# Kernel optimization log

Measured on AMD Instinct MI355X. Metric: run time of the kernel, lower is better.

Reference implementation:

```python
import jax, jax.numpy as jnp
import numpy as np

B = 2048          # batch (vmapped samples)
STEPS = 64        # hardcoded scan length in module
H = 64            # hidden_size
W = 128           # width_size
NZ = 32           # noise_size (control_size)
INZ = 32          # initial_noise_size
D = 8             # data_size


def lipswish(x):
    return 0.909 * jax.nn.silu(x)


def _mlp3(x, W0, b0, W1, b1, W2, b2, act, final_act):
    # eqx.nn.MLP with depth=2: in->width, width->width, width->out
    h = act(x @ W0.T + b0)
    h = act(h @ W1.T + b1)
    return final_act(h @ W2.T + b2)


def setup_inputs() -> dict:
    key = jax.random.key(0)
    ks = jax.random.split(key, 32)

    def lin(k, out_d, in_d):
        lim = 1.0 / np.sqrt(in_d)
        kw, kb = jax.random.split(k)
        Wm = jax.random.uniform(kw, (out_d, in_d), minval=-lim, maxval=lim, dtype=jnp.float32)
        bv = jax.random.uniform(kb, (out_d,), minval=-lim, maxval=lim, dtype=jnp.float32)
        return Wm, bv

    Wi0, bi0 = lin(ks[0], W, INZ)
    Wi1, bi1 = lin(ks[1], W, W)
    Wi2, bi2 = lin(ks[2], H, W)

    Wv0, bv0 = lin(ks[3], W, H + 1)
    Wv1, bv1 = lin(ks[4], W, W)
    Wv2, bv2 = lin(ks[5], H, W)
    scale_v = jax.random.uniform(ks[6], (H,), minval=0.9, maxval=1.1, dtype=jnp.float32)

    Wc0, bc0 = lin(ks[7], W, H + 1)
    Wc1, bc1 = lin(ks[8], W, W)
    Wc2, bc2 = lin(ks[9], H * NZ, W)
    scale_c = jax.random.uniform(ks[10], (H, NZ), minval=0.9, maxval=1.1, dtype=jnp.float32)

    Wr, br = lin(ks[11], D, H)

    ts = jnp.arange(STEPS + 1, dtype=jnp.float32)
    init_noise = jax.random.normal(ks[12], (B, INZ), dtype=jnp.float32)
    bm = jax.random.normal(ks[13], (B, STEPS, NZ), dtype=jnp.float32)

    return dict(ts=ts, init_noise=init_noise, bm=bm,
                Wi0=Wi0, bi0=bi0, Wi1=Wi1, bi1=bi1, Wi2=Wi2, bi2=bi2,
                scale_v=scale_v, Wv0=Wv0, bv0=bv0, Wv1=Wv1, bv1=bv1, Wv2=Wv2, bv2=bv2,
                scale_c=scale_c, Wc0=Wc0, bc0=bc0, Wc1=Wc1, bc1=bc1, Wc2=Wc2, bc2=bc2,
                Wr=Wr, br=br)


def reference(ts, init_noise, bm,
              Wi0, bi0, Wi1, bi1, Wi2, bi2,
              scale_v, Wv0, bv0, Wv1, bv1, Wv2, bv2,
              scale_c, Wc0, bc0, Wc1, bc1, Wc2, bc2,
              Wr, br):
    t0 = ts[0]
    dt = jnp.float32(1.0)  # dt0 hardcoded in module
    sqrt_dt = jnp.sqrt(dt)

    # initial MLP (relu hidden, identity final): noise -> y0 [B,H]
    y0 = _mlp3(init_noise, Wi0, bi0, Wi1, bi1, Wi2, bi2, jax.nn.relu, lambda x: x)

    bm_t = jnp.transpose(bm, (1, 0, 2))  # [STEPS, B, NZ]
    idx = jnp.arange(STEPS, dtype=jnp.float32)

    def step(y, xs):
        i, bm_i = xs
        t = t0 + i * dt
        tcol = jnp.broadcast_to(jnp.reshape(t, (1, 1)), (y.shape[0], 1))
        inp = jnp.concatenate([tcol, y], axis=1)  # [B, H+1]
        # drift vector field
        drift = scale_v * _mlp3(inp, Wv0, bv0, Wv1, bv1, Wv2, bv2, lipswish, jnp.tanh)
        # controlled vector field: [B, H, NZ]
        diff = scale_c * _mlp3(inp, Wc0, bc0, Wc1, bc1, Wc2, bc2, lipswish, jnp.tanh).reshape(-1, H, NZ)
        y1 = y + drift * dt + jnp.einsum('bhn,bn->bh', diff, bm_i * sqrt_dt)
        return y1, y1

    _, ys = jax.lax.scan(step, y0, (idx, bm_t), length=STEPS, unroll=8)  # ys [STEPS,B,H]
    out = jnp.einsum('tbh,dh->tbd', ys, Wr) + br  # readout per step
    return jnp.transpose(out, (1, 0, 2))  # [B, STEPS, D]
```

## Files before the change

kernel.cpp:

```cpp
#include <hip/hip_runtime.h>
#include <stdint.h>
#include <stddef.h>


typedef __attribute__((ext_vector_type(8))) short bf16x8;
typedef __attribute__((ext_vector_type(4))) float f32x4;
typedef __attribute__((ext_vector_type(2))) float f32x2;
typedef __attribute__((ext_vector_type(4))) int   i32x4;

#define BB 16
#define NWG 256

#define WS_WI0 0
#define WS_WI1 8192
#define WS_WI2 40960
#define WS_WV0 57344
#define WS_WV1 73728
#define WS_WV2 106496
#define WS_WC0 122880
#define WS_WC1 139264
#define WS_WC2 172032
#define WS_TV0 696320
#define WS_TC0 696832
#define WS_XCHG 700416
#define WS_FLAG 2273280

#define LD_WV0 0
#define LD_WV1 16384
#define LD_WC0 49152
#define LD_WC1 65536
#define LD_YBF 98304
#define LD_H1V 100352
#define LD_H1C 104448
#define LD_H2V 108544
#define LD_H2C 112640
#define LD_Y   116736
#define LD_DB  121088
#define LD_BM  125440
#define LD_BSC 127552
#define LD_BEV 135744
#define LD_BEC 136256
#define LD_BV1 136768
#define LD_BC1 137280
#define LD_BV2 137792
#define LD_SV  138048
#define LD_WR  138304
#define LD_BR  140480
#define LDS_TOTAL 140512

__device__ __forceinline__ short f2bf(float f) {
  uint32_t u = __builtin_bit_cast(uint32_t, f);
  uint32_t r = (u + 0x7fffu + ((u >> 16) & 1u)) >> 16;
  return (short)r;
}
__device__ __forceinline__ float bf2f(short s) {
  uint32_t u = ((uint32_t)(uint16_t)s) << 16;
  return __builtin_bit_cast(float, u);
}
__device__ __forceinline__ float tanh_fast(float x) {
  float e = __builtin_amdgcn_exp2f(x * 2.8853900817779268f);
  return __builtin_fmaf(-2.f, __builtin_amdgcn_rcpf(e + 1.f), 1.f);
}
__device__ __forceinline__ float lipswish(float x) {
  float s = __builtin_amdgcn_rcpf(1.f + __builtin_amdgcn_exp2f(-1.4426950408889634f * x));
  return 0.909f * x * s;
}
__device__ __forceinline__ float red16(float x) {
  int v;
  v = __builtin_amdgcn_update_dpp(0, __builtin_bit_cast(int, x), 0xB1, 0xF, 0xF, true);
  x += __builtin_bit_cast(float, v);
  v = __builtin_amdgcn_update_dpp(0, __builtin_bit_cast(int, x), 0x4E, 0xF, 0xF, true);
  x += __builtin_bit_cast(float, v);
  v = __builtin_amdgcn_update_dpp(0, __builtin_bit_cast(int, x), 0x141, 0xF, 0xF, true);
  x += __builtin_bit_cast(float, v);
  v = __builtin_amdgcn_update_dpp(0, __builtin_bit_cast(int, x), 0x140, 0xF, 0xF, true);
  x += __builtin_bit_cast(float, v);
  return x;
}
__device__ __forceinline__ float red4(float x) {
  int v;
  v = __builtin_amdgcn_update_dpp(0, __builtin_bit_cast(int, x), 0xB1, 0xF, 0xF, true);
  x += __builtin_bit_cast(float, v);
  v = __builtin_amdgcn_update_dpp(0, __builtin_bit_cast(int, x), 0x4E, 0xF, 0xF, true);
  x += __builtin_bit_cast(float, v);
  return x;
}
__device__ __forceinline__ void write_act(char* buf, int m, int k, short v) {
  int addr = ((k >> 5) << 10) + (m + ((k >> 3) & 3) * 16) * 16 + ((k & 7) << 1);
  *(short*)(buf + addr) = v;
}

template<int KF>
__device__ __forceinline__ f32x4 gemm_tile(const char* abase, const char* bbase, int lane) {
  f32x4 acc = {0.f, 0.f, 0.f, 0.f};
#pragma unroll
  for (int k = 0; k < KF; k++) {
    bf16x8 a = *(const bf16x8*)(abase + k * 1024 + lane * 16);
    bf16x8 b = *(const bf16x8*)(bbase + k * 1024 + lane * 16);
    acc = __builtin_amdgcn_mfma_f32_16x16x32_bf16(a, b, acc, 0, 0, 0);
  }
  return acc;
}

__global__ __launch_bounds__(256) void prep_kernel(
    const float* Wi0, const float* Wi1, const float* Wi2,
    const float* Wv0, const float* Wv1, const float* Wv2,
    const float* Wc0, const float* Wc1, const float* Wc2, char* ws) {
  int gid = blockIdx.x * 256 + threadIdx.x;
  if (gid < 512) ((unsigned*)(ws + WS_FLAG))[gid] = 0;
  if (gid < 680 * 64) {
    int frag = gid >> 6, lane = gid & 63;
    const float* src; int start, KI, srcK, c0;
    if      (frag < 8)   { src = Wi0; start = 0;   KI = 1; srcK = 32;  c0 = 0; }
    else if (frag < 40)  { src = Wi1; start = 8;   KI = 4; srcK = 128; c0 = 0; }
    else if (frag < 56)  { src = Wi2; start = 40;  KI = 4; srcK = 128; c0 = 0; }
    else if (frag < 72)  { src = Wv0; start = 56;  KI = 2; srcK = 65;  c0 = 1; }
    else if (frag < 104) { src = Wv1; start = 72;  KI = 4; srcK = 128; c0 = 0; }
    else if (frag < 120) { src = Wv2; start = 104; KI = 4; srcK = 128; c0 = 0; }
    else if (frag < 136) { src = Wc0; start = 120; KI = 2; srcK = 65;  c0 = 1; }
    else if (frag < 168) { src = Wc1; start = 136; KI = 4; srcK = 128; c0 = 0; }
    else                 { src = Wc2; start = 168; KI = 4; srcK = 128; c0 = 0; }
    int rel = frag - start;
    int nt = rel / KI, ki = rel % KI;
    int n16 = lane & 15, quad = lane >> 4;
    const float* s = src + (nt * 16 + n16) * srcK + c0 + ki * 32 + quad * 8;
    bf16x8 v;
#pragma unroll
    for (int j = 0; j < 8; j++) v[j] = f2bf(s[j]);
    *(bf16x8*)(ws + (size_t)frag * 1024 + lane * 16) = v;
  } else {
    int i = gid - 680 * 64;
    if (i < 128)      ((float*)(ws + WS_TV0))[i] = Wv0[i * 65];
    else if (i < 256) ((float*)(ws + WS_TC0))[i - 128] = Wc0[(i - 128) * 65];
  }
}

__global__ __launch_bounds__(512, 2)
void sde_kernel(
    const float* ts, const float* init_noise, const float* bm,
    const float* bi0, const float* bi1, const float* bi2,
    const float* bv0, const float* bv1, const float* bv2, const float* scale_v,
    const float* bc0, const float* bc1, const float* bc2, const float* scale_c,
    const float* Wr, const float* br,
    char* ws, float* out) {
  extern __shared__ __align__(16) char lds[];
  const int tid  = threadIdx.x;
  const int lane = tid & 63;
  const int wv   = tid >> 6;
  const int nl   = lane & 15;
  const int quad = lane >> 4;
  const int bid  = blockIdx.x;
  const int ro   = (bid >> 3) & 1;
  const int pid  = ((bid >> 4) << 3) | (bid & 7);
  const int b0   = pid * BB;
  const int hbase = ro << 5;
  const char* wc2 = ws + WS_WC2 + (size_t)(ro * 64 + wv * 8) * 4096;
  char* xch = ws + WS_XCHG;
  unsigned* flags = (unsigned*)(ws + WS_FLAG);
  const int myflag = (pid << 1) | ro;
  const int paflag = (pid << 1) | (1 - ro);

  bf16x8 vf0 = {}, vf1 = {}, vf2 = {}, vf3 = {};
  if (wv < 2) {
    const char* vb = ws + WS_WV2 + (size_t)(ro * 2 + wv) * 4096;
    vf0 = *(const bf16x8*)(vb +    0 + lane * 16);
    vf1 = *(const bf16x8*)(vb + 1024 + lane * 16);
    vf2 = *(const bf16x8*)(vb + 2048 + lane * 16);
    vf3 = *(const bf16x8*)(vb + 3072 + lane * 16);
  }
  float tvq = 0.f, bbq = 0.f;
  if (tid >= 256) {
    int j = tid - 256;
    if (j < 128) { tvq = ((const float*)(ws + WS_TV0))[j];       bbq = bv0[j]; }
    else         { tvq = ((const float*)(ws + WS_TC0))[j - 128]; bbq = bc0[j - 128]; }
  }

  {
    const i32x4* s0 = (const i32x4*)(ws + WS_WV0);
    const i32x4* s1 = (const i32x4*)(ws + WS_WC0);
    i32x4* d0 = (i32x4*)(lds + LD_WV0);
    i32x4* d1 = (i32x4*)(lds + LD_WC0);
    for (int j = tid; j < 3072; j += 512) { d0[j] = s0[j]; d1[j] = s1[j]; }
  }
  for (int j = tid; j < 2048; j += 512) {
    uint32_t u = (uint32_t)(uint16_t)f2bf(bc2[j]) |
                 ((uint32_t)(uint16_t)f2bf(scale_c[j]) << 16);
    ((uint32_t*)(lds + LD_BSC))[j] = u;
  }
  if (tid < 128)      { ((float*)(lds + LD_BV1))[tid] = bv1[tid];
                        ((float*)(lds + LD_BC1))[tid] = bc1[tid]; }
  else if (tid < 192) { int k = tid - 128; ((float*)(lds + LD_BV2))[k] = bv2[k];
                        ((float*)(lds + LD_SV))[k] = scale_v[k]; }
  else if (tid < 200) { int k = tid - 192; ((float*)(lds + LD_BR))[k] = br[k]; }
  { int dd = tid >> 6, k = tid & 63;
    ((float*)(lds + LD_WR))[dd * 68 + k] = Wr[dd * 64 + k]; }
  { int m = tid >> 5, k = tid & 31;
    write_act(lds + LD_YBF, m, k, f2bf(init_noise[(b0 + m) * 32 + k])); }
  __syncthreads();

  { f32x4 acc = gemm_tile<1>(lds + LD_YBF, ws + WS_WI0 + wv * 1024, lane);
    int col = wv * 16 + nl; float bias = bi0[col];
#pragma unroll
    for (int r = 0; r < 4; r++)
      write_act(lds + LD_H1V, quad * 4 + r, col, f2bf(fmaxf(0.f, acc[r] + bias))); }
  __syncthreads();
  { f32x4 acc = gemm_tile<4>(lds + LD_H1V, ws + WS_WI1 + wv * 4096, lane);
    int col = wv * 16 + nl; float bias = bi1[col];
#pragma unroll
    for (int r = 0; r < 4; r++)
      write_act(lds + LD_H2V, quad * 4 + r, col, f2bf(fmaxf(0.f, acc[r] + bias))); }
  __syncthreads();
  if (wv < 4) {
    f32x4 acc = gemm_tile<4>(lds + LD_H2V, ws + WS_WI2 + wv * 4096, lane);
    int col = wv * 16 + nl; float bias = bi2[col];
#pragma unroll
    for (int r = 0; r < 4; r++)
      ((float*)(lds + LD_Y))[(quad * 4 + r) * 68 + col] = acc[r] + bias;
  }
  __syncthreads();

  const float ts0 = ts[0];
  for (int e = tid; e < 1024; e += 512) {
    int row = e >> 6, k = e & 63;
    write_act(lds + LD_YBF, row, k, f2bf(((float*)(lds + LD_Y))[row * 68 + k]));
  }
  ((float*)(lds + LD_BM))[(tid >> 5) * 33 + (tid & 31)] =
      bm[((size_t)(b0 + (tid >> 5)) * 64 + 0) * 32 + (tid & 31)];
  if (tid >= 256) {
    int j = tid - 256; float v = bbq + ts0 * tvq;
    if (j < 128) ((float*)(lds + LD_BEV))[j] = v;
    else         ((float*)(lds + LD_BEC))[j - 128] = v;
  }
  __syncthreads();

  for (int step = 0; step < 64; step++) {
    {
      int col = wv * 16 + nl;
      f32x4 av = gemm_tile<2>(lds + LD_YBF, lds + LD_WV0 + wv * 2048, lane);
      f32x4 ac = gemm_tile<2>(lds + LD_YBF, lds + LD_WC0 + wv * 2048, lane);
      float bv = ((float*)(lds + LD_BEV))[col];
      float bc = ((float*)(lds + LD_BEC))[col];
#pragma unroll
      for (int r = 0; r < 4; r++) {
        write_act(lds + LD_H1V, quad * 4 + r, col, f2bf(lipswish(av[r] + bv)));
        write_act(lds + LD_H1C, quad * 4 + r, col, f2bf(lipswish(ac[r] + bc)));
      }
    }
    __syncthreads();
    bf16x8 bE0 = *(const bf16x8*)(wc2 +    0 + lane * 16);
    bf16x8 bE1 = *(const bf16x8*)(wc2 + 1024 + lane * 16);
    bf16x8 bE2 = *(const bf16x8*)(wc2 + 2048 + lane * 16);
    bf16x8 bE3 = *(const bf16x8*)(wc2 + 3072 + lane * 16);
    bf16x8 bO0 = *(const bf16x8*)(wc2 + 4096 +    0 + lane * 16);
    bf16x8 bO1 = *(const bf16x8*)(wc2 + 4096 + 1024 + lane * 16);
    bf16x8 bO2 = *(const bf16x8*)(wc2 + 4096 + 2048 + lane * 16);
    bf16x8 bO3 = *(const bf16x8*)(wc2 + 4096 + 3072 + lane * 16);
    {
      int col = wv * 16 + nl;
      f32x4 av = gemm_tile<4>(lds + LD_H1V, lds + LD_WV1 + wv * 4096, lane);
      f32x4 ac = gemm_tile<4>(lds + LD_H1C, lds + LD_WC1 + wv * 4096, lane);
      float bv = ((float*)(lds + LD_BV1))[col];
      float bc = ((float*)(lds + LD_BC1))[col];
#pragma unroll
      for (int r = 0; r < 4; r++) {
        write_act(lds + LD_H2V, quad * 4 + r, col, f2bf(lipswish(av[r] + bv)));
        write_act(lds + LD_H2C, quad * 4 + r, col, f2bf(lipswish(ac[r] + bc)));
      }
    }
    __syncthreads();
    float bm_next = 0.f;
    if (step + 1 < 64)
      bm_next = bm[((size_t)(b0 + (tid >> 5)) * 64 + (step + 1)) * 32 + (tid & 31)];
    if (wv < 2) {
      f32x4 acc = {0.f, 0.f, 0.f, 0.f};
      acc = __builtin_amdgcn_mfma_f32_16x16x32_bf16(
          *(const bf16x8*)(lds + LD_H2V +    0 + lane * 16), vf0, acc, 0, 0, 0);
      acc = __builtin_amdgcn_mfma_f32_16x16x32_bf16(
          *(const bf16x8*)(lds + LD_H2V + 1024 + lane * 16), vf1, acc, 0, 0, 0);
      acc = __builtin_amdgcn_mfma_f32_16x16x32_bf16(
          *(const bf16x8*)(lds + LD_H2V + 2048 + lane * 16), vf2, acc, 0, 0, 0);
      acc = __builtin_amdgcn_mfma_f32_16x16x32_bf16(
          *(const bf16x8*)(lds + LD_H2V + 3072 + lane * 16), vf3, acc, 0, 0, 0);
      int col = (ro * 2 + wv) * 16 + nl;
      float bias = ((float*)(lds + LD_BV2))[col];
      float sv   = ((float*)(lds + LD_SV))[col];
#pragma unroll
      for (int r = 0; r < 4; r++)
        ((float*)(lds + LD_DB))[(quad * 4 + r) * 68 + col] = sv * tanh_fast(acc[r] + bias);
    }
    {
      bf16x8 a0f = *(const bf16x8*)(lds + LD_H2C +    0 + lane * 16);
      bf16x8 a1f = *(const bf16x8*)(lds + LD_H2C + 1024 + lane * 16);
      bf16x8 a2f = *(const bf16x8*)(lds + LD_H2C + 2048 + lane * 16);
      bf16x8 a3f = *(const bf16x8*)(lds + LD_H2C + 3072 + lane * 16);
      const float* bmp = (const float*)(lds + LD_BM);
      float bmr00 = bmp[(quad * 4 + 0) * 33 + nl];
      float bmr01 = bmp[(quad * 4 + 1) * 33 + nl];
      float bmr02 = bmp[(quad * 4 + 2) * 33 + nl];
      float bmr03 = bmp[(quad * 4 + 3) * 33 + nl];
      float bmr10 = bmp[(quad * 4 + 0) * 33 + 16 + nl];
      float bmr11 = bmp[(quad * 4 + 1) * 33 + 16 + nl];
      float bmr12 = bmp[(quad * 4 + 2) * 33 + 16 + nl];
      float bmr13 = bmp[(quad * 4 + 3) * 33 + 16 + nl];
      const uint32_t* bscp = (const uint32_t*)(lds + LD_BSC) + (ro * 64 + wv * 8) * 16 + nl;
      float ps0, ps1, ps2, ps3;

#define DIFF_PAIR(P)                                                          \
      {                                                     \
        f32x4 acc = {0.f, 0.f, 0.f, 0.f};                                     \
        acc = __builtin_amdgcn_mfma_f32_16x16x32_bf16(a0f, bE0, acc, 0, 0, 0);\
        acc = __builtin_amdgcn_mfma_f32_16x16x32_bf16(a1f, bE1, acc, 0, 0, 0);\
        acc = __builtin_amdgcn_mfma_f32_16x16x32_bf16(a2f, bE2, acc, 0, 0, 0);\
        acc = __builtin_amdgcn_mfma_f32_16x16x32_bf16(a3f, bE3, acc, 0, 0, 0);\
        if ((P) < 3) {                                                        \
          bE0 = *(const bf16x8*)(wc2 + (2*(P)+2)*4096 +    0 + lane*16);      \
          bE1 = *(const bf16x8*)(wc2 + (2*(P)+2)*4096 + 1024 + lane*16);      \
          bE2 = *(const bf16x8*)(wc2 + (2*(P)+2)*4096 + 2048 + lane*16);      \
          bE3 = *(const bf16x8*)(wc2 + (2*(P)+2)*4096 + 3072 + lane*16);      \
        }                                                                     \
        uint32_t bsc = bscp[(2*(P))*16];                                      \
        float bc2v = bf2f((short)(bsc & 0xffffu));                            \
        float scv  = bf2f((short)(bsc >> 16));                                \
        ps0 = tanh_fast(acc[0] + bc2v) * scv * bmr00;                         \
        ps1 = tanh_fast(acc[1] + bc2v) * scv * bmr01;                         \
        ps2 = tanh_fast(acc[2] + bc2v) * scv * bmr02;                         \
        ps3 = tanh_fast(acc[3] + bc2v) * scv * bmr03;                         \
      }                                                                       \
      {                                                    \
        f32x4 acc = {0.f, 0.f, 0.f, 0.f};                                     \
        acc = __builtin_amdgcn_mfma_f32_16x16x32_bf16(a0f, bO0, acc, 0, 0, 0);\
        acc = __builtin_amdgcn_mfma_f32_16x16x32_bf16(a1f, bO1, acc, 0, 0, 0);\
        acc = __builtin_amdgcn_mfma_f32_16x16x32_bf16(a2f, bO2, acc, 0, 0, 0);\
        acc = __builtin_amdgcn_mfma_f32_16x16x32_bf16(a3f, bO3, acc, 0, 0, 0);\
        if ((P) < 3) {                                                        \
          bO0 = *(const bf16x8*)(wc2 + (2*(P)+3)*4096 +    0 + lane*16);      \
          bO1 = *(const bf16x8*)(wc2 + (2*(P)+3)*4096 + 1024 + lane*16);      \
          bO2 = *(const bf16x8*)(wc2 + (2*(P)+3)*4096 + 2048 + lane*16);      \
          bO3 = *(const bf16x8*)(wc2 + (2*(P)+3)*4096 + 3072 + lane*16);      \
        }                                                                     \
        uint32_t bsc = bscp[(2*(P)+1)*16];                                    \
        float bc2v = bf2f((short)(bsc & 0xffffu));                            \
        float scv  = bf2f((short)(bsc >> 16));                                \
        ps0 += tanh_fast(acc[0] + bc2v) * scv * bmr10;                        \
        ps1 += tanh_fast(acc[1] + bc2v) * scv * bmr11;                        \
        ps2 += tanh_fast(acc[2] + bc2v) * scv * bmr12;                        \
        ps3 += tanh_fast(acc[3] + bc2v) * scv * bmr13;                        \
        ps0 = red16(ps0); ps1 = red16(ps1); ps2 = red16(ps2); ps3 = red16(ps3);\
        if (nl < 4) {                                                         \
          int row = quad * 4 + nl;                                            \
          float s = (nl == 0) ? ps0 : (nl == 1) ? ps1 : (nl == 2) ? ps2 : ps3;\
          ((float*)(lds + LD_Y))[row * 68 + (hbase + (wv << 2) + (P))] += s;  \
        }                                                                     \
      }

      DIFF_PAIR(0)
      DIFF_PAIR(1)
      DIFF_PAIR(2)
      DIFF_PAIR(3)
#undef DIFF_PAIR
    }
    __syncthreads();
    char* my_slot = xch + (size_t)(((myflag << 1) | (step & 1))) * 3072;
    const char* pa_slot = xch + (size_t)(((paflag << 1) | (step & 1))) * 3072;
    if (tid < 128) {
      int row = tid >> 3, kq = tid & 7;
      int c0 = hbase + kq * 4;
      f32x4 yv = *(const f32x4*)(lds + LD_Y  + (row * 68 + c0) * 4);
      f32x4 db = *(const f32x4*)(lds + LD_DB + (row * 68 + c0) * 4);
      f32x4 vn = yv + db;
      *(f32x4*)(lds + LD_Y + (row * 68 + c0) * 4) = vn;
      uint32_t p0 = (uint32_t)(uint16_t)f2bf(vn[0]) | ((uint32_t)(uint16_t)f2bf(vn[1]) << 16);
      uint32_t p1 = (uint32_t)(uint16_t)f2bf(vn[2]) | ((uint32_t)(uint16_t)f2bf(vn[3]) << 16);
      uint64_t p64 = (uint64_t)p0 | ((uint64_t)p1 << 32);
      int inner = (row + (kq >> 1) * 16) * 16 + ((kq & 1) << 3);
      *(uint64_t*)(lds + LD_YBF + ro * 1024 + inner) = p64;
      unsigned long long* pbf = (unsigned long long*)(my_slot);
      unsigned long long* pf  = (unsigned long long*)(my_slot + 1024);
      __hip_atomic_store(pbf + (inner >> 3), (unsigned long long)p64,
                         __ATOMIC_RELAXED, __HIP_MEMORY_SCOPE_AGENT);
      f32x2 lo = {vn[0], vn[1]}, hi = {vn[2], vn[3]};
      __hip_atomic_store(pf + 2 * tid,     __builtin_bit_cast(unsigned long long, lo),
                         __ATOMIC_RELAXED, __HIP_MEMORY_SCOPE_AGENT);
      __hip_atomic_store(pf + 2 * tid + 1, __builtin_bit_cast(unsigned long long, hi),
                         __ATOMIC_RELAXED, __HIP_MEMORY_SCOPE_AGENT);
    } else if (tid >= 256 && step + 1 < 64) {
      int j = tid - 256; float v = bbq + (ts0 + (float)(step + 1)) * tvq;
      if (j < 128) ((float*)(lds + LD_BEV))[j] = v;
      else         ((float*)(lds + LD_BEC))[j - 128] = v;
    }
    if (step + 1 < 64)
      ((float*)(lds + LD_BM))[(tid >> 5) * 33 + (tid & 31)] = bm_next;
    asm volatile("s_waitcnt vmcnt(0)" ::: "memory");
    __syncthreads();
    if (tid == 0) {
      __hip_atomic_store(flags + myflag, (unsigned)(step + 1),
                         __ATOMIC_RELAXED, __HIP_MEMORY_SCOPE_AGENT);
      unsigned want = (unsigned)(step + 1);
      int guard = 0;
      while (__hip_atomic_load(flags + paflag, __ATOMIC_RELAXED,
                               __HIP_MEMORY_SCOPE_AGENT) < want) {
        __builtin_amdgcn_s_sleep(2);
        if (++guard > (1 << 20)) break;
      }
    }
    __syncthreads();
    if (tid < 128) {
      const unsigned long long* qbf = (const unsigned long long*)(pa_slot);
      const unsigned long long* qf  = (const unsigned long long*)(pa_slot + 1024);
      unsigned long long v = __hip_atomic_load(qbf + tid, __ATOMIC_RELAXED,
                                               __HIP_MEMORY_SCOPE_AGENT);
      *(unsigned long long*)(lds + LD_YBF + (1 - ro) * 1024 + tid * 8) = v;
      unsigned long long a = __hip_atomic_load(qf + 2 * tid, __ATOMIC_RELAXED,
                                               __HIP_MEMORY_SCOPE_AGENT);
      unsigned long long b = __hip_atomic_load(qf + 2 * tid + 1, __ATOMIC_RELAXED,
                                               __HIP_MEMORY_SCOPE_AGENT);
      int row = tid >> 3, kq = tid & 7;
      char* yd = lds + LD_Y + (row * 68 + ((1 - ro) << 5) + kq * 4) * 4;
      *(unsigned long long*)(yd)     = a;
      *(unsigned long long*)(yd + 8) = b;
    }
    __syncthreads();
    {
      int row = ro * 8 + wv;
      int dd  = lane >> 3;
      int kg  = lane & 7;
      const float* yr = (const float*)(lds + LD_Y) + row * 68;
      const float* wr = (const float*)(lds + LD_WR) + dd * 68;
      float s = 0.f;
#pragma unroll
      for (int i = 0; i < 8; i++) s = fmaf(yr[kg + 8 * i], wr[kg + 8 * i], s);
      s = red4(s);
      s += __shfl_xor(s, 4, 64);
      if (kg == 0)
        out[(size_t)(b0 + row) * 512 + step * 8 + dd] =
            s + ((const float*)(lds + LD_BR))[dd];
    }
  }
}

extern "C" void kernel_launch(void* const* d_in, const int* in_sizes, int n_in,
                              void* d_out, int out_size, void* d_ws, size_t ws_size,
                              hipStream_t stream) {
  (void)in_sizes; (void)n_in; (void)out_size; (void)ws_size;
  const float* ts         = (const float*)d_in[0];
  const float* init_noise = (const float*)d_in[1];
  const float* bm         = (const float*)d_in[2];
  const float* Wi0 = (const float*)d_in[3];
  const float* bi0 = (const float*)d_in[4];
  const float* Wi1 = (const float*)d_in[5];
  const float* bi1 = (const float*)d_in[6];
  const float* Wi2 = (const float*)d_in[7];
  const float* bi2 = (const float*)d_in[8];
  const float* scale_v = (const float*)d_in[9];
  const float* Wv0 = (const float*)d_in[10];
  const float* bv0 = (const float*)d_in[11];
  const float* Wv1 = (const float*)d_in[12];
  const float* bv1 = (const float*)d_in[13];
  const float* Wv2 = (const float*)d_in[14];
  const float* bv2 = (const float*)d_in[15];
  const float* scale_c = (const float*)d_in[16];
  const float* Wc0 = (const float*)d_in[17];
  const float* bc0 = (const float*)d_in[18];
  const float* Wc1 = (const float*)d_in[19];
  const float* bc1 = (const float*)d_in[20];
  const float* Wc2 = (const float*)d_in[21];
  const float* bc2 = (const float*)d_in[22];
  const float* Wr  = (const float*)d_in[23];
  const float* br  = (const float*)d_in[24];
  char*  ws  = (char*)d_ws;
  float* out = (float*)d_out;

  hipFuncSetAttribute((const void*)sde_kernel,
                      hipFuncAttributeMaxDynamicSharedMemorySize, LDS_TOTAL);

  prep_kernel<<<171, 256, 0, stream>>>(Wi0, Wi1, Wi2, Wv0, Wv1, Wv2, Wc0, Wc1, Wc2, ws);
  sde_kernel<<<NWG, 512, LDS_TOTAL, stream>>>(
      ts, init_noise, bm, bi0, bi1, bi2, bv0, bv1, bv2, scale_v,
      bc0, bc1, bc2, scale_c, Wr, br, ws, out);
}
```

Before: 494.8 us.

## Exchange partial readout sums and use per-wave flags to cut barriers

Each half-workgroup now computes a partial readout dot product over its own 32 hidden columns and sends only those partials, instead of its fp32 half of y, to the partner workgroup, which shrinks the exchange slot. Each wave signals readiness with its own flag, and the 128 threads that read the exchange spin on a 64-bit pair of partner flags. This removes the single-thread flag spin and two block-wide barriers per step, along with the separate readout phase. In exchange, the partner's fp32 half of y is no longer copied into LD_Y, so correctness depends on nothing else reading those columns. The finer-grained spinning also adds more polling traffic.

```diff
diff --git a/kernel.cpp b/kernel.cpp
--- a/kernel.cpp
+++ b/kernel.cpp
@@ -5,7 +5,6 @@
 
 typedef __attribute__((ext_vector_type(8))) short bf16x8;
 typedef __attribute__((ext_vector_type(4))) float f32x4;
-typedef __attribute__((ext_vector_type(2))) float f32x2;
 typedef __attribute__((ext_vector_type(4))) int   i32x4;
 
 #define BB 16
@@ -74,14 +73,6 @@
   v = __builtin_amdgcn_update_dpp(0, __builtin_bit_cast(int, x), 0x141, 0xF, 0xF, true);
   x += __builtin_bit_cast(float, v);
   v = __builtin_amdgcn_update_dpp(0, __builtin_bit_cast(int, x), 0x140, 0xF, 0xF, true);
-  x += __builtin_bit_cast(float, v);
-  return x;
-}
-__device__ __forceinline__ float red4(float x) {
-  int v;
-  v = __builtin_amdgcn_update_dpp(0, __builtin_bit_cast(int, x), 0xB1, 0xF, 0xF, true);
-  x += __builtin_bit_cast(float, v);
-  v = __builtin_amdgcn_update_dpp(0, __builtin_bit_cast(int, x), 0x4E, 0xF, 0xF, true);
   x += __builtin_bit_cast(float, v);
   return x;
 }
@@ -159,6 +150,7 @@
   unsigned* flags = (unsigned*)(ws + WS_FLAG);
   const int myflag = (pid << 1) | ro;
   const int paflag = (pid << 1) | (1 - ro);
+  const float brv = (tid < 128) ? br[tid & 7] : 0.f;
 
   bf16x8 vf0 = {}, vf1 = {}, vf2 = {}, vf3 = {};
   if (wv < 2) {
@@ -360,8 +352,9 @@
 #undef DIFF_PAIR
     }
     __syncthreads();
-    char* my_slot = xch + (size_t)(((myflag << 1) | (step & 1))) * 3072;
-    const char* pa_slot = xch + (size_t)(((paflag << 1) | (step & 1))) * 3072;
+    char* my_slot = xch + (size_t)(((myflag << 1) | (step & 1))) * 2048;
+    const char* pa_slot = xch + (size_t)(((paflag << 1) | (step & 1))) * 2048;
+    float part = 0.f;
     if (tid < 128) {
       int row = tid >> 3, kq = tid & 7;
       int c0 = hbase + kq * 4;
@@ -374,15 +367,25 @@
       uint64_t p64 = (uint64_t)p0 | ((uint64_t)p1 << 32);
       int inner = (row + (kq >> 1) * 16) * 16 + ((kq & 1) << 3);
       *(uint64_t*)(lds + LD_YBF + ro * 1024 + inner) = p64;
-      unsigned long long* pbf = (unsigned long long*)(my_slot);
-      unsigned long long* pf  = (unsigned long long*)(my_slot + 1024);
-      __hip_atomic_store(pbf + (inner >> 3), (unsigned long long)p64,
+      __hip_atomic_store((unsigned long long*)(my_slot + inner), (unsigned long long)p64,
                          __ATOMIC_RELAXED, __HIP_MEMORY_SCOPE_AGENT);
-      f32x2 lo = {vn[0], vn[1]}, hi = {vn[2], vn[3]};
-      __hip_atomic_store(pf + 2 * tid,     __builtin_bit_cast(unsigned long long, lo),
-                         __ATOMIC_RELAXED, __HIP_MEMORY_SCOPE_AGENT);
-      __hip_atomic_store(pf + 2 * tid + 1, __builtin_bit_cast(unsigned long long, hi),
-                         __ATOMIC_RELAXED, __HIP_MEMORY_SCOPE_AGENT);
+      const float* yr = (const float*)(lds + LD_Y) + row * 68 + hbase;
+      const float* wr = (const float*)(lds + LD_WR) + kq * 68 + hbase;
+#pragma unroll
+      for (int j = 0; j < 8; j++) {
+        f32x4 a = *(const f32x4*)(yr + j * 4);
+        f32x4 w = *(const f32x4*)(wr + j * 4);
+        part = fmaf(a[0], w[0], part); part = fmaf(a[1], w[1], part);
+        part = fmaf(a[2], w[2], part); part = fmaf(a[3], w[3], part);
+      }
+      if ((tid >> 6) != ro)
+        __hip_atomic_store((unsigned*)(my_slot + 1024) + (tid & 63),
+                           __builtin_bit_cast(unsigned, part),
+                           __ATOMIC_RELAXED, __HIP_MEMORY_SCOPE_AGENT);
+      asm volatile("s_waitcnt vmcnt(0)" ::: "memory");
+      if (lane == 0)
+        __hip_atomic_store(flags + ((myflag << 1) | (tid >> 6)), (unsigned)(step + 1),
+                           __ATOMIC_RELAXED, __HIP_MEMORY_SCOPE_AGENT);
     } else if (tid >= 256 && step + 1 < 64) {
       int j = tid - 256; float v = bbq + (ts0 + (float)(step + 1)) * tvq;
       if (j < 128) ((float*)(lds + LD_BEV))[j] = v;
@@ -390,51 +393,29 @@
     }
     if (step + 1 < 64)
       ((float*)(lds + LD_BM))[(tid >> 5) * 33 + (tid & 31)] = bm_next;
-    asm volatile("s_waitcnt vmcnt(0)" ::: "memory");
+    if (tid < 128) {
+      unsigned want = (unsigned)(step + 1);
+      const unsigned long long* pfl = (const unsigned long long*)(flags + (paflag << 1));
+      int guard = 0;
+      for (;;) {
+        unsigned long long fv = __hip_atomic_load(pfl, __ATOMIC_RELAXED,
+                                                  __HIP_MEMORY_SCOPE_AGENT);
+        if ((unsigned)fv >= want && (unsigned)(fv >> 32) >= want) break;
+        __builtin_amdgcn_s_sleep(1);
+        if (++guard > (1 << 20)) break;
+      }
+      unsigned long long v = __hip_atomic_load((const unsigned long long*)pa_slot + tid,
+                                               __ATOMIC_RELAXED, __HIP_MEMORY_SCOPE_AGENT);
+      *(unsigned long long*)(lds + LD_YBF + (1 - ro) * 1024 + tid * 8) = v;
+      if ((tid >> 6) == ro) {
+        float pp = __builtin_bit_cast(float, __hip_atomic_load(
+            (const unsigned*)(pa_slot + 1024) + (tid & 63),
+            __ATOMIC_RELAXED, __HIP_MEMORY_SCOPE_AGENT));
+        int row = tid >> 3, dd = tid & 7;
+        out[(size_t)(b0 + row) * 512 + step * 8 + dd] = part + pp + brv;
+      }
+    }
     __syncthreads();
-    if (tid == 0) {
-      __hip_atomic_store(flags + myflag, (unsigned)(step + 1),
-                         __ATOMIC_RELAXED, __HIP_MEMORY_SCOPE_AGENT);
-      unsigned want = (unsigned)(step + 1);
-      int guard = 0;
-      while (__hip_atomic_load(flags + paflag, __ATOMIC_RELAXED,
-                               __HIP_MEMORY_SCOPE_AGENT) < want) {
-        __builtin_amdgcn_s_sleep(2);
-        if (++guard > (1 << 20)) break;
-      }
-    }
-    __syncthreads();
-    if (tid < 128) {
-      const unsigned long long* qbf = (const unsigned long long*)(pa_slot);
-      const unsigned long long* qf  = (const unsigned long long*)(pa_slot + 1024);
-      unsigned long long v = __hip_atomic_load(qbf + tid, __ATOMIC_RELAXED,
-                                               __HIP_MEMORY_SCOPE_AGENT);
-      *(unsigned long long*)(lds + LD_YBF + (1 - ro) * 1024 + tid * 8) = v;
-      unsigned long long a = __hip_atomic_load(qf + 2 * tid, __ATOMIC_RELAXED,
-                                               __HIP_MEMORY_SCOPE_AGENT);
-      unsigned long long b = __hip_atomic_load(qf + 2 * tid + 1, __ATOMIC_RELAXED,
-                                               __HIP_MEMORY_SCOPE_AGENT);
-      int row = tid >> 3, kq = tid & 7;
-      char* yd = lds + LD_Y + (row * 68 + ((1 - ro) << 5) + kq * 4) * 4;
-      *(unsigned long long*)(yd)     = a;
-      *(unsigned long long*)(yd + 8) = b;
-    }
-    __syncthreads();
-    {
-      int row = ro * 8 + wv;
-      int dd  = lane >> 3;
-      int kg  = lane & 7;
-      const float* yr = (const float*)(lds + LD_Y) + row * 68;
-      const float* wr = (const float*)(lds + LD_WR) + dd * 68;
-      float s = 0.f;
-#pragma unroll
-      for (int i = 0; i < 8; i++) s = fmaf(yr[kg + 8 * i], wr[kg + 8 * i], s);
-      s = red4(s);
-      s += __shfl_xor(s, 4, 64);
-      if (kg == 0)
-        out[(size_t)(b0 + row) * 512 + step * 8 + dd] =
-            s + ((const float*)(lds + LD_BR))[dd];
-    }
   }
 }
 
```

Measured after the change: 510.1 us. 3.1% more time.
